# Performance work log

Hardware: AMD Instinct MI355X
Metric: run time of the kernel (lower is better)

The kernel has to match this reference:

```python
import jax, jax.numpy as jnp
import numpy as np

N, X_DIM, Y_DIM, HID = 1024, 256, 256, 256  # HID = hidden_size // 2


def setup_inputs() -> dict:
    key = jax.random.key(0)
    ks = jax.random.split(key, 11)
    s_in = 1.0 / np.sqrt(X_DIM)
    s_h = 1.0 / np.sqrt(HID)
    return {
        "x_samples": jax.random.normal(ks[0], (N, X_DIM), jnp.float32),
        "y_samples": jax.random.normal(ks[1], (N, Y_DIM), jnp.float32),
        "z_samples": jax.random.normal(ks[2], (N, Y_DIM), jnp.float32),
        "w1_mu": jax.random.uniform(ks[3], (HID, X_DIM), jnp.float32, -s_in, s_in),
        "b1_mu": jax.random.uniform(ks[4], (HID,), jnp.float32, -s_in, s_in),
        "w2_mu": jax.random.uniform(ks[5], (Y_DIM, HID), jnp.float32, -s_h, s_h),
        "b2_mu": jax.random.uniform(ks[6], (Y_DIM,), jnp.float32, -s_h, s_h),
        "w1_lv": jax.random.uniform(ks[7], (HID, X_DIM), jnp.float32, -s_in, s_in),
        "b1_lv": jax.random.uniform(ks[8], (HID,), jnp.float32, -s_in, s_in),
        "w2_lv": jax.random.uniform(ks[9], (Y_DIM, HID), jnp.float32, -s_h, s_h),
        "b2_lv": jax.random.uniform(ks[10], (Y_DIM,), jnp.float32, -s_h, s_h),
    }


def reference(x_samples, y_samples, z_samples,
              w1_mu, b1_mu, w2_mu, b2_mu,
              w1_lv, b1_lv, w2_lv, b2_lv):
    # MLP heads (torch Linear: x @ W.T + b)
    h_mu = jax.nn.relu(x_samples @ w1_mu.T + b1_mu)
    mu = h_mu @ w2_mu.T + b2_mu                       # [N, D]
    h_lv = jax.nn.relu(x_samples @ w1_lv.T + b1_lv)
    logvar = jnp.tanh(h_lv @ w2_lv.T + b2_lv)          # [N, D]

    inv2var = 1.0 / (2.0 * jnp.exp(logvar))           # [N, D]

    # positive: per-sample conditional log-density term
    positive = -((mu - y_samples) ** 2 + (mu - z_samples) ** 2) * inv2var  # [N, D]

    # negative: mean over all pairings (i: prediction, j: sample)
    # pairwise squared diffs materialize [N, N, D] like the original broadcast
    pred = mu[:, None, :]                              # [N, 1, D]
    sq = (y_samples[None, :, :] - pred) ** 2 + (z_samples[None, :, :] - pred) ** 2
    negative = -sq.mean(axis=1) * inv2var              # [N, D]

    return jax.nn.relu(positive.sum(axis=-1) - negative.sum(axis=-1)).mean()
```

## Files before the change

### kernel.cpp

```cpp
#include <hip/hip_runtime.h>
#include <math.h>

constexpr int LSK = 264;

typedef short bf16x8 __attribute__((ext_vector_type(8)));
typedef float f32x4  __attribute__((ext_vector_type(4)));

__device__ __forceinline__ unsigned short f2bf_rne(float f) {
    unsigned u = __float_as_uint(f);
    unsigned r = (u + 0x7fff + ((u >> 16) & 1)) >> 16;
    return (unsigned short)r;
}
__device__ __forceinline__ float bf2f(unsigned short h) {
    return __uint_as_float(((unsigned)h) << 16);
}
__device__ __forceinline__ void split4(float4 v, ushort4& hi, ushort4& lo) {
    hi.x = f2bf_rne(v.x); lo.x = f2bf_rne(v.x - bf2f(hi.x));
    hi.y = f2bf_rne(v.y); lo.y = f2bf_rne(v.y - bf2f(hi.y));
    hi.z = f2bf_rne(v.z); lo.z = f2bf_rne(v.z - bf2f(hi.z));
    hi.w = f2bf_rne(v.w); lo.w = f2bf_rne(v.w - bf2f(hi.w));
}

__global__ __launch_bounds__(256, 2)
void k1_layer1(const float* __restrict__ x,
               const float* __restrict__ w1m, const float* __restrict__ w1l,
               const float* __restrict__ b1m, const float* __restrict__ b1l,
               const float* __restrict__ w2m, const float* __restrict__ w2l,
               unsigned short* __restrict__ hmH, unsigned short* __restrict__ hmL,
               unsigned short* __restrict__ hlH, unsigned short* __restrict__ hlL,
               unsigned short* __restrict__ w2mH, unsigned short* __restrict__ w2mL,
               unsigned short* __restrict__ w2lH, unsigned short* __restrict__ w2lL,
               const float* __restrict__ y, const float* __restrict__ z,
               float* __restrict__ pA1, float* __restrict__ pB1,
               float* __restrict__ rowAcc) {
    const int bid = blockIdx.x, t = threadIdx.x;

    const int head = bid & 1, ct = (bid >> 1) & 7, rt = bid >> 4;
    const int rowBase = rt * 32, colBase = ct * 32;
    const int w = t >> 6, lane = t & 63, quad = lane >> 4, mr = lane & 15;
    const int mt = w & 1, nt = w >> 1;

    const float* Bw   = head ? w1l : w1m;
    const float* bias = head ? b1l : b1m;
    unsigned short* CH = head ? hlH : hmH;
    unsigned short* CL = head ? hlL : hmL;

    __shared__ __align__(16) unsigned short Ah[32][LSK], Al[32][LSK];
    __shared__ __align__(16) unsigned short Bh[32][LSK], Bl[32][LSK];

#pragma unroll
    for (int p = 0; p < 8; p++) {
        int idx = p * 256 + t;
        int r = idx >> 6, k4 = idx & 63;
        float4 av = *(const float4*)&x [(rowBase + r) * 256 + k4 * 4];
        float4 bv = *(const float4*)&Bw[(colBase + r) * 256 + k4 * 4];
        ushort4 h4, l4;
        split4(av, h4, l4);
        *(ushort4*)&Ah[r][k4 * 4] = h4;
        *(ushort4*)&Al[r][k4 * 4] = l4;
        split4(bv, h4, l4);
        *(ushort4*)&Bh[r][k4 * 4] = h4;
        *(ushort4*)&Bl[r][k4 * 4] = l4;
    }
    __syncthreads();

    const unsigned short* aHp = &Ah[mt * 16 + mr][0];
    const unsigned short* aLp = &Al[mt * 16 + mr][0];
    const unsigned short* bHp = &Bh[nt * 16 + mr][0];
    const unsigned short* bLp = &Bl[nt * 16 + mr][0];

    f32x4 acc = {0.f, 0.f, 0.f, 0.f};
#pragma unroll
    for (int ks = 0; ks < 8; ks++) {
        int ko = ks * 32 + quad * 8;
        bf16x8 ah = *(const bf16x8*)&aHp[ko];
        bf16x8 al = *(const bf16x8*)&aLp[ko];
        bf16x8 bh = *(const bf16x8*)&bHp[ko];
        bf16x8 bl = *(const bf16x8*)&bLp[ko];
        acc = __builtin_amdgcn_mfma_f32_16x16x32_bf16(ah, bh, acc, 0, 0, 0);
        acc = __builtin_amdgcn_mfma_f32_16x16x32_bf16(ah, bl, acc, 0, 0, 0);
        acc = __builtin_amdgcn_mfma_f32_16x16x32_bf16(al, bh, acc, 0, 0, 0);
    }

    {
        int cg = colBase + nt * 16 + mr;
        float bb = bias[cg];
#pragma unroll
        for (int reg = 0; reg < 4; reg++) {
            int rg = rowBase + mt * 16 + quad * 4 + reg;
            float v = fmaxf(acc[reg] + bb, 0.f);
            unsigned short hi = f2bf_rne(v);
            CH[rg * 256 + cg] = hi;
            CL[rg * 256 + cg] = f2bf_rne(v - bf2f(hi));
        }
    }

    if (bid < 256) {
        int off = bid * 256 + t;
        float vm = w2m[off], vl = w2l[off];
        unsigned short h1 = f2bf_rne(vm);
        w2mH[off] = h1; w2mL[off] = f2bf_rne(vm - bf2f(h1));
        unsigned short h2 = f2bf_rne(vl);
        w2lH[off] = h2; w2lL[off] = f2bf_rne(vl - bf2f(h2));
    }

    if (bid < 64) {
        float sA = 0.f, sB = 0.f;
        int base = bid * 16 * 256 + t;
#pragma unroll 4
        for (int j = 0; j < 16; j++) {
            float yv = y[base + j * 256];
            float zv = z[base + j * 256];
            sA += yv * yv + zv * zv;
            sB += yv + zv;
        }
        pA1[bid * 256 + t] = sA;
        pB1[bid * 256 + t] = sB;
    }

    if (bid < 4) rowAcc[bid * 256 + t] = 0.f;
}

constexpr int LSB = 72;

__global__ __launch_bounds__(256, 2)
void k2_fused(const unsigned short* __restrict__ hmH, const unsigned short* __restrict__ hmL,
              const unsigned short* __restrict__ hlH, const unsigned short* __restrict__ hlL,
              const unsigned short* __restrict__ w2mH, const unsigned short* __restrict__ w2mL,
              const unsigned short* __restrict__ w2lH, const unsigned short* __restrict__ w2lL,
              const float* __restrict__ b2m, const float* __restrict__ b2l,
              const float* __restrict__ y, const float* __restrict__ z,
              const float* __restrict__ pA1, const float* __restrict__ pB1,
              float* __restrict__ rowAcc) {
    const int bid = blockIdx.x, t = threadIdx.x;
    const int rt = bid >> 4, ct = bid & 15;
    const int rowBase = rt * 32, colBase = ct * 16;
    const int w = t >> 6, lane = t & 63, quad = lane >> 4, mr = lane & 15;
    const int h = w & 1, mt = w >> 1;

    __shared__ __align__(16) unsigned short Ast[2][2][32][LSB];
    __shared__ __align__(16) unsigned short Bst[2][2][16][LSB];
    __shared__ float Cx[2][32][17];
    __shared__ float partA[16][16], partB[16][16];
    __shared__ float mAf[16], mBf[16];

    const unsigned short* Aarr[4] = {hmH, hmL, hlH, hlL};
    const unsigned short* Barr[4] = {w2mH, w2mL, w2lH, w2lL};

    {
        int s = t >> 4, c = t & 15;
        float a0 = 0.f, b0 = 0.f;
#pragma unroll
        for (int j = 0; j < 4; j++) {
            a0 += pA1[(s * 4 + j) * 256 + colBase + c];
            b0 += pB1[(s * 4 + j) * 256 + colBase + c];
        }
        partA[s][c] = a0;
        partB[s][c] = b0;
    }
    __syncthreads();
    if (t < 16) {
        float sA = 0.f, sB = 0.f;
#pragma unroll
        for (int s = 0; s < 16; s++) { sA += partA[s][t]; sB += partB[s][t]; }
        mAf[t] = sA * (1.f / 1024.f);
        mBf[t] = sB * (1.f / 1024.f);
    }

    f32x4 acc = {0.f, 0.f, 0.f, 0.f};

    for (int kt = 0; kt < 256; kt += 64) {
#pragma unroll
        for (int hp = 0; hp < 4; hp++) {
#pragma unroll
            for (int p = 0; p < 2; p++) {
                int idx = p * 256 + t;
                int r = idx >> 4, k4 = idx & 15;
                *(ushort4*)&Ast[hp >> 1][hp & 1][r][k4 * 4] =
                    *(const ushort4*)&Aarr[hp][(rowBase + r) * 256 + kt + k4 * 4];
            }
            {
                int r = t >> 4, k4 = t & 15;
                *(ushort4*)&Bst[hp >> 1][hp & 1][r][k4 * 4] =
                    *(const ushort4*)&Barr[hp][(colBase + r) * 256 + kt + k4 * 4];
            }
        }
        __syncthreads();

#pragma unroll
        for (int kk = 0; kk < 64; kk += 32) {
            int ko = kk + quad * 8;
            bf16x8 ah = *(const bf16x8*)&Ast[h][0][mt * 16 + mr][ko];
            bf16x8 al = *(const bf16x8*)&Ast[h][1][mt * 16 + mr][ko];
            bf16x8 bh = *(const bf16x8*)&Bst[h][0][mr][ko];
            bf16x8 bl = *(const bf16x8*)&Bst[h][1][mr][ko];
            acc = __builtin_amdgcn_mfma_f32_16x16x32_bf16(ah, bh, acc, 0, 0, 0);
            acc = __builtin_amdgcn_mfma_f32_16x16x32_bf16(ah, bl, acc, 0, 0, 0);
            acc = __builtin_amdgcn_mfma_f32_16x16x32_bf16(al, bh, acc, 0, 0, 0);
        }
        __syncthreads();
    }

    {
        const float* bias = h ? b2l : b2m;
        float bb = bias[colBase + mr];
#pragma unroll
        for (int reg = 0; reg < 4; reg++)
            Cx[h][mt * 16 + quad * 4 + reg][mr] = acc[reg] + bb;
    }
    __syncthreads();

    {
        int col = t & 15, rg = t >> 4;
        int gcol = colBase + col;
        float mA = mAf[col], mB = mBf[col];
#pragma unroll
        for (int rr = 0; rr < 2; rr++) {
            int row = rg * 2 + rr;
            int o = (rowBase + row) * 256 + gcol;
            float m  = Cx[0][row][col];
            float lv = tanhf(Cx[1][row][col]);
            float iv = 0.5f * expf(-lv);
            float yv = y[o];
            float zv = z[o];
            float Mt = mA - 2.f * m * mB + 2.f * m * m;
            float dy = m - yv, dz = m - zv;
            float term = iv * (Mt - dy * dy - dz * dz);
#pragma unroll
            for (int msk = 8; msk; msk >>= 1)
                term += __shfl_xor(term, msk, 16);
            if (col == 0) atomicAdd(&rowAcc[rowBase + row], term);
        }
    }
}

__global__ __launch_bounds__(256)
void k3_final(const float* __restrict__ rowAcc, float* __restrict__ out) {
    __shared__ float red[4];
    int t = threadIdx.x, lane = t & 63, wave = t >> 6;
    float v = 0.f;
#pragma unroll
    for (int p = 0; p < 4; p++)
        v += fmaxf(rowAcc[p * 256 + t], 0.f);
#pragma unroll
    for (int msk = 32; msk; msk >>= 1)
        v += __shfl_xor(v, msk, 64);
    if (lane == 0) red[wave] = v;
    __syncthreads();
    if (t == 0)
        out[0] = (red[0] + red[1] + red[2] + red[3]) * (1.f / 1024.f);
}

extern "C" void kernel_launch(void* const* d_in, const int* in_sizes, int n_in,
                              void* d_out, int out_size, void* d_ws, size_t ws_size,
                              hipStream_t stream) {
    const float* x   = (const float*)d_in[0];
    const float* y   = (const float*)d_in[1];
    const float* zs  = (const float*)d_in[2];
    const float* w1m = (const float*)d_in[3];
    const float* b1m = (const float*)d_in[4];
    const float* w2m = (const float*)d_in[5];
    const float* b2m = (const float*)d_in[6];
    const float* w1l = (const float*)d_in[7];
    const float* b1l = (const float*)d_in[8];
    const float* w2l = (const float*)d_in[9];
    const float* b2l = (const float*)d_in[10];
    float* out = (float*)d_out;

    char* ws = (char*)d_ws;
    float* pA1    = (float*)(ws);
    float* pB1    = (float*)(ws + (256u << 10));
    float* rowAcc = (float*)(ws + (512u << 10));
    unsigned short* hmH = (unsigned short*)(ws + (1024u << 10));
    unsigned short* hmL = (unsigned short*)(ws + (1536u << 10));
    unsigned short* hlH = (unsigned short*)(ws + (2048u << 10));
    unsigned short* hlL = (unsigned short*)(ws + (2560u << 10));
    unsigned short* w2mH = (unsigned short*)(ws + (3072u << 10));
    unsigned short* w2mL = (unsigned short*)(ws + (3200u << 10));
    unsigned short* w2lH = (unsigned short*)(ws + (3328u << 10));
    unsigned short* w2lL = (unsigned short*)(ws + (3456u << 10));

    k1_layer1<<<512, 256, 0, stream>>>(x, w1m, w1l, b1m, b1l, w2m, w2l,
                                       hmH, hmL, hlH, hlL,
                                       w2mH, w2mL, w2lH, w2lL,
                                       y, zs, pA1, pB1, rowAcc);
    k2_fused<<<512, 256, 0, stream>>>(hmH, hmL, hlH, hlL,
                                      w2mH, w2mL, w2lH, w2lL,
                                      b2m, b2l, y, zs, pA1, pB1, rowAcc);
    k3_final<<<1, 256, 0, stream>>>(rowAcc, out);
}
```

Measured before the change: 91.44 us.

## Double-buffer layer-2 GEMM loads and split W2 to bf16 inside k2

k1 no longer pre-splits W2 into hi/lo bf16 arrays. k2 instead reads fp32 W2 directly and splits it into hi/lo while staging it into shared memory. k2's K loop now uses register prefetch with double-buffered shared tiles, which removes one barrier per iteration and overlaps global loads with MFMA work. The y/z column-sum partials move to the last 128 blocks of k1, each covering 8 rows instead of 16. The trade-off is that every k2 block redoes the W2 split and shared-memory use doubles, which may reduce occupancy.

```diff
diff --git a/kernel.cpp b/kernel.cpp
--- a/kernel.cpp
+++ b/kernel.cpp
@@ -2,6 +2,7 @@
 #include <math.h>
 
 constexpr int LSK = 264;
+constexpr int LSB = 72;
 
 typedef short bf16x8 __attribute__((ext_vector_type(8)));
 typedef float f32x4  __attribute__((ext_vector_type(4)));
@@ -25,11 +26,8 @@
 void k1_layer1(const float* __restrict__ x,
                const float* __restrict__ w1m, const float* __restrict__ w1l,
                const float* __restrict__ b1m, const float* __restrict__ b1l,
-               const float* __restrict__ w2m, const float* __restrict__ w2l,
                unsigned short* __restrict__ hmH, unsigned short* __restrict__ hmL,
                unsigned short* __restrict__ hlH, unsigned short* __restrict__ hlL,
-               unsigned short* __restrict__ w2mH, unsigned short* __restrict__ w2mL,
-               unsigned short* __restrict__ w2lH, unsigned short* __restrict__ w2lL,
                const float* __restrict__ y, const float* __restrict__ z,
                float* __restrict__ pA1, float* __restrict__ pB1,
                float* __restrict__ rowAcc) {
@@ -47,6 +45,21 @@
 
     __shared__ __align__(16) unsigned short Ah[32][LSK], Al[32][LSK];
     __shared__ __align__(16) unsigned short Bh[32][LSK], Bl[32][LSK];
+
+    if (bid >= 384) {
+        int m = bid - 384;
+        float sA = 0.f, sB = 0.f;
+        int base = m * 8 * 256 + t;
+#pragma unroll
+        for (int j = 0; j < 8; j++) {
+            float yv = y[base + j * 256];
+            float zv = z[base + j * 256];
+            sA += yv * yv + zv * zv;
+            sB += yv + zv;
+        }
+        pA1[m * 256 + t] = sA;
+        pB1[m * 256 + t] = sB;
+    }
 
 #pragma unroll
     for (int p = 0; p < 8; p++) {
@@ -95,39 +108,13 @@
         }
     }
 
-    if (bid < 256) {
-        int off = bid * 256 + t;
-        float vm = w2m[off], vl = w2l[off];
-        unsigned short h1 = f2bf_rne(vm);
-        w2mH[off] = h1; w2mL[off] = f2bf_rne(vm - bf2f(h1));
-        unsigned short h2 = f2bf_rne(vl);
-        w2lH[off] = h2; w2lL[off] = f2bf_rne(vl - bf2f(h2));
-    }
-
-    if (bid < 64) {
-        float sA = 0.f, sB = 0.f;
-        int base = bid * 16 * 256 + t;
-#pragma unroll 4
-        for (int j = 0; j < 16; j++) {
-            float yv = y[base + j * 256];
-            float zv = z[base + j * 256];
-            sA += yv * yv + zv * zv;
-            sB += yv + zv;
-        }
-        pA1[bid * 256 + t] = sA;
-        pB1[bid * 256 + t] = sB;
-    }
-
     if (bid < 4) rowAcc[bid * 256 + t] = 0.f;
 }
-
-constexpr int LSB = 72;
 
 __global__ __launch_bounds__(256, 2)
 void k2_fused(const unsigned short* __restrict__ hmH, const unsigned short* __restrict__ hmL,
               const unsigned short* __restrict__ hlH, const unsigned short* __restrict__ hlL,
-              const unsigned short* __restrict__ w2mH, const unsigned short* __restrict__ w2mL,
-              const unsigned short* __restrict__ w2lH, const unsigned short* __restrict__ w2lL,
+              const float* __restrict__ w2m, const float* __restrict__ w2l,
               const float* __restrict__ b2m, const float* __restrict__ b2l,
               const float* __restrict__ y, const float* __restrict__ z,
               const float* __restrict__ pA1, const float* __restrict__ pB1,
@@ -138,75 +125,93 @@
     const int w = t >> 6, lane = t & 63, quad = lane >> 4, mr = lane & 15;
     const int h = w & 1, mt = w >> 1;
 
-    __shared__ __align__(16) unsigned short Ast[2][2][32][LSB];
-    __shared__ __align__(16) unsigned short Bst[2][2][16][LSB];
+    __shared__ __align__(16) unsigned short Ast[2][2][2][32][LSB];
+    __shared__ __align__(16) unsigned short Bst[2][2][2][16][LSB];
     __shared__ float Cx[2][32][17];
     __shared__ float partA[16][16], partB[16][16];
     __shared__ float mAf[16], mBf[16];
 
     const unsigned short* Aarr[4] = {hmH, hmL, hlH, hlL};
-    const unsigned short* Barr[4] = {w2mH, w2mL, w2lH, w2lL};
 
     {
         int s = t >> 4, c = t & 15;
         float a0 = 0.f, b0 = 0.f;
 #pragma unroll
-        for (int j = 0; j < 4; j++) {
-            a0 += pA1[(s * 4 + j) * 256 + colBase + c];
-            b0 += pB1[(s * 4 + j) * 256 + colBase + c];
+        for (int j = 0; j < 8; j++) {
+            a0 += pA1[(s * 8 + j) * 256 + colBase + c];
+            b0 += pB1[(s * 8 + j) * 256 + colBase + c];
         }
         partA[s][c] = a0;
         partB[s][c] = b0;
     }
-    __syncthreads();
+
+    ushort4 pa[8]; float4 pb[2];
+    const int ar_r[2] = { (t + 0) >> 4, (t + 256) >> 4 };
+    const int ar_k = t & 15;
+    const int br_r = t >> 4;
+
+#define K2_LOAD(ktv)                                                          \
+    {                                                                         \
+        int kb = (ktv);                                                       \
+        _Pragma("unroll")                                                     \
+        for (int ar = 0; ar < 4; ar++) {                                      \
+            pa[ar * 2 + 0] = *(const ushort4*)&Aarr[ar][(rowBase + ar_r[0]) * 256 + kb + ar_k * 4]; \
+            pa[ar * 2 + 1] = *(const ushort4*)&Aarr[ar][(rowBase + ar_r[1]) * 256 + kb + ar_k * 4]; \
+        }                                                                     \
+        pb[0] = *(const float4*)&w2m[(colBase + br_r) * 256 + kb + ar_k * 4]; \
+        pb[1] = *(const float4*)&w2l[(colBase + br_r) * 256 + kb + ar_k * 4]; \
+    }
+
+    K2_LOAD(0);
+
+    f32x4 acc = {0.f, 0.f, 0.f, 0.f};
+
+    for (int kt4 = 0; kt4 < 4; kt4++) {
+        int buf = kt4 & 1;
+#pragma unroll
+        for (int ar = 0; ar < 4; ar++) {
+            *(ushort4*)&Ast[buf][ar >> 1][ar & 1][ar_r[0]][ar_k * 4] = pa[ar * 2 + 0];
+            *(ushort4*)&Ast[buf][ar >> 1][ar & 1][ar_r[1]][ar_k * 4] = pa[ar * 2 + 1];
+        }
+        {
+            ushort4 h4, l4;
+            split4(pb[0], h4, l4);
+            *(ushort4*)&Bst[buf][0][0][br_r][ar_k * 4] = h4;
+            *(ushort4*)&Bst[buf][0][1][br_r][ar_k * 4] = l4;
+            split4(pb[1], h4, l4);
+            *(ushort4*)&Bst[buf][1][0][br_r][ar_k * 4] = h4;
+            *(ushort4*)&Bst[buf][1][1][br_r][ar_k * 4] = l4;
+        }
+        if (kt4 < 3) K2_LOAD((kt4 + 1) * 64);
+        __syncthreads();
+
+#pragma unroll
+        for (int kk = 0; kk < 64; kk += 32) {
+            int ko = kk + quad * 8;
+            bf16x8 ah = *(const bf16x8*)&Ast[buf][h][0][mt * 16 + mr][ko];
+            bf16x8 al = *(const bf16x8*)&Ast[buf][h][1][mt * 16 + mr][ko];
+            bf16x8 bh = *(const bf16x8*)&Bst[buf][h][0][mr][ko];
+            bf16x8 bl = *(const bf16x8*)&Bst[buf][h][1][mr][ko];
+            acc = __builtin_amdgcn_mfma_f32_16x16x32_bf16(ah, bh, acc, 0, 0, 0);
+            acc = __builtin_amdgcn_mfma_f32_16x16x32_bf16(ah, bl, acc, 0, 0, 0);
+            acc = __builtin_amdgcn_mfma_f32_16x16x32_bf16(al, bh, acc, 0, 0, 0);
+        }
+    }
+#undef K2_LOAD
+
+    {
+        const float* bias = h ? b2l : b2m;
+        float bb = bias[colBase + mr];
+#pragma unroll
+        for (int reg = 0; reg < 4; reg++)
+            Cx[h][mt * 16 + quad * 4 + reg][mr] = acc[reg] + bb;
+    }
     if (t < 16) {
         float sA = 0.f, sB = 0.f;
 #pragma unroll
         for (int s = 0; s < 16; s++) { sA += partA[s][t]; sB += partB[s][t]; }
         mAf[t] = sA * (1.f / 1024.f);
         mBf[t] = sB * (1.f / 1024.f);
-    }
-
-    f32x4 acc = {0.f, 0.f, 0.f, 0.f};
-
-    for (int kt = 0; kt < 256; kt += 64) {
-#pragma unroll
-        for (int hp = 0; hp < 4; hp++) {
-#pragma unroll
-            for (int p = 0; p < 2; p++) {
-                int idx = p * 256 + t;
-                int r = idx >> 4, k4 = idx & 15;
-                *(ushort4*)&Ast[hp >> 1][hp & 1][r][k4 * 4] =
-                    *(const ushort4*)&Aarr[hp][(rowBase + r) * 256 + kt + k4 * 4];
-            }
-            {
-                int r = t >> 4, k4 = t & 15;
-                *(ushort4*)&Bst[hp >> 1][hp & 1][r][k4 * 4] =
-                    *(const ushort4*)&Barr[hp][(colBase + r) * 256 + kt + k4 * 4];
-            }
-        }
-        __syncthreads();
-
-#pragma unroll
-        for (int kk = 0; kk < 64; kk += 32) {
-            int ko = kk + quad * 8;
-            bf16x8 ah = *(const bf16x8*)&Ast[h][0][mt * 16 + mr][ko];
-            bf16x8 al = *(const bf16x8*)&Ast[h][1][mt * 16 + mr][ko];
-            bf16x8 bh = *(const bf16x8*)&Bst[h][0][mr][ko];
-            bf16x8 bl = *(const bf16x8*)&Bst[h][1][mr][ko];
-            acc = __builtin_amdgcn_mfma_f32_16x16x32_bf16(ah, bh, acc, 0, 0, 0);
-            acc = __builtin_amdgcn_mfma_f32_16x16x32_bf16(ah, bl, acc, 0, 0, 0);
-            acc = __builtin_amdgcn_mfma_f32_16x16x32_bf16(al, bh, acc, 0, 0, 0);
-        }
-        __syncthreads();
-    }
-
-    {
-        const float* bias = h ? b2l : b2m;
-        float bb = bias[colBase + mr];
-#pragma unroll
-        for (int reg = 0; reg < 4; reg++)
-            Cx[h][mt * 16 + quad * 4 + reg][mr] = acc[reg] + bb;
     }
     __syncthreads();
 
@@ -275,17 +280,12 @@
     unsigned short* hmL = (unsigned short*)(ws + (1536u << 10));
     unsigned short* hlH = (unsigned short*)(ws + (2048u << 10));
     unsigned short* hlL = (unsigned short*)(ws + (2560u << 10));
-    unsigned short* w2mH = (unsigned short*)(ws + (3072u << 10));
-    unsigned short* w2mL = (unsigned short*)(ws + (3200u << 10));
-    unsigned short* w2lH = (unsigned short*)(ws + (3328u << 10));
-    unsigned short* w2lL = (unsigned short*)(ws + (3456u << 10));
-
-    k1_layer1<<<512, 256, 0, stream>>>(x, w1m, w1l, b1m, b1l, w2m, w2l,
+
+    k1_layer1<<<512, 256, 0, stream>>>(x, w1m, w1l, b1m, b1l,
                                        hmH, hmL, hlH, hlL,
-                                       w2mH, w2mL, w2lH, w2lL,
                                        y, zs, pA1, pB1, rowAcc);
     k2_fused<<<512, 256, 0, stream>>>(hmH, hmL, hlH, hlL,
-                                      w2mH, w2mL, w2lH, w2lL,
-                                      b2m, b2l, y, zs, pA1, pB1, rowAcc);
+                                      w2m, w2l, b2m, b2l,
+                                      y, zs, pA1, pB1, rowAcc);
     k3_final<<<1, 256, 0, stream>>>(rowAcc, out);
 }
```

New measurement: 90.82 us. No clear change (-0.7%).
